# Optimization experiments

Hardware: AMD Instinct MI355X
Metric: run time of the kernel (lower is better)

Reference implementation:

```python
import jax, jax.numpy as jnp
import numpy as np

V, D, H, F, L, B, T = 32000, 512, 8, 2048, 4, 4, 1024
DK = D // H
S = 0.02  # init scale


def setup_inputs() -> dict:
    key = jax.random.key(0)
    ks = jax.random.split(key, 10)
    inp = {
        'x': jax.random.randint(ks[0], (B, T), 0, V),
        'embed': jax.random.normal(ks[1], (V, D), jnp.float32) * S,
        'Wq': jax.random.normal(ks[2], (L, D, D), jnp.float32) * S,
        'bq': jnp.zeros((L, D), jnp.float32),
        'Wk': jax.random.normal(ks[3], (L, D, D), jnp.float32) * S,
        'bk': jnp.zeros((L, D), jnp.float32),
        'Wv': jax.random.normal(ks[4], (L, D, D), jnp.float32) * S,
        'bv': jnp.zeros((L, D), jnp.float32),
        'Wo': jax.random.normal(ks[5], (L, D, D), jnp.float32) * S,
        'bo': jnp.zeros((L, D), jnp.float32),
        'ln1_s': jnp.ones((L, D), jnp.float32),
        'ln1_b': jnp.zeros((L, D), jnp.float32),
        'W1': jax.random.normal(ks[6], (L, D, F), jnp.float32) * S,
        'b1': jnp.zeros((L, F), jnp.float32),
        'W2': jax.random.normal(ks[7], (L, F, D), jnp.float32) * S,
        'b2': jnp.zeros((L, D), jnp.float32),
        'ln2_s': jnp.ones((L, D), jnp.float32),
        'ln2_b': jnp.zeros((L, D), jnp.float32),
        'lnf_s': jnp.ones((D,), jnp.float32),
        'lnf_b': jnp.zeros((D,), jnp.float32),
        'Wl': jax.random.normal(ks[8], (D, V), jnp.float32) * S,
        'bl': jnp.zeros((V,), jnp.float32),
    }
    return inp


def _layernorm(x, s, b, eps=1e-5):
    m = jnp.mean(x, axis=-1, keepdims=True)
    v = jnp.mean(jnp.square(x - m), axis=-1, keepdims=True)
    return (x - m) * jax.lax.rsqrt(v + eps) * s + b


def _forward(x, embed, Wq, bq, Wk, bk, Wv, bv, Wo, bo, ln1_s, ln1_b,
             W1, b1, W2, b2, ln2_s, ln2_b, lnf_s, lnf_b, Wl, bl):
    Bb, Tt = x.shape
    emb = embed.at[0].set(0.0)  # padding_idx = 0
    h = emb[x]  # [B,T,D]
    # sinusoidal positional encoding
    pos = jnp.arange(Tt, dtype=jnp.float32)[:, None]
    div = jnp.exp(jnp.arange(0, D, 2, dtype=jnp.float32) * (-np.log(10000.0) / D))
    pe = jnp.zeros((Tt, D), jnp.float32)
    pe = pe.at[:, 0::2].set(jnp.sin(pos * div)).at[:, 1::2].set(jnp.cos(pos * div))
    h = h + pe[None]
    # additive causal mask: 0 on/below diag, -inf above
    causal = jnp.triu(jnp.full((Tt, Tt), -jnp.inf, jnp.float32), 1)
    scale = 1.0 / np.sqrt(DK)
    for l in range(L):
        q = (h @ Wq[l] + bq[l]).reshape(Bb, Tt, H, DK)
        k = (h @ Wk[l] + bk[l]).reshape(Bb, Tt, H, DK)
        v = (h @ Wv[l] + bv[l]).reshape(Bb, Tt, H, DK)
        scores = jnp.einsum('bqhd,bkhd->bhqk', q, k) * scale + causal
        attn = jax.nn.softmax(scores, axis=-1)  # dropout=0 -> identity
        o = jnp.einsum('bhqk,bkhd->bqhd', attn, v).reshape(Bb, Tt, D)
        o = o @ Wo[l] + bo[l]
        h = _layernorm(h + o, ln1_s[l], ln1_b[l])
        ff = jax.nn.gelu(h @ W1[l] + b1[l], approximate=False) @ W2[l] + b2[l]
        h = _layernorm(h + ff, ln2_s[l], ln2_b[l])
    h = _layernorm(h, lnf_s, lnf_b)
    return h @ Wl + bl  # [B,T,V] logits


def reference(x, embed, Wq, bq, Wk, bk, Wv, bv, Wo, bo, ln1_s, ln1_b,
              W1, b1, W2, b2, ln2_s, ln2_b, lnf_s, lnf_b, Wl, bl):
    return _forward(x, embed, Wq, bq, Wk, bk, Wv, bv, Wo, bo, ln1_s, ln1_b,
                    W1, b1, W2, b2, ln2_s, ln2_b, lnf_s, lnf_b, Wl, bl)
```

## Files before the change

### kernel.cpp

```cpp
#include <hip/hip_runtime.h>
#include <math.h>

#define Mtot 4096
#define Dd   512
#define Hh   8
#define DKk  64
#define TT   1024
#define Ff   2048
#define Ll   4
#define Vv   32000

typedef __attribute__((ext_vector_type(8))) short bf16x8;
typedef __attribute__((ext_vector_type(4))) float f32x4;
typedef unsigned short u16;

__device__ __forceinline__ u16 f2b(float f) {
    union { float f; unsigned u; } x; x.f = f;
    unsigned r = x.u + 0x7fffu + ((x.u >> 16) & 1u);
    return (u16)(r >> 16);
}

typedef const __attribute__((address_space(1))) unsigned int* gp_t;
typedef __attribute__((address_space(3))) unsigned int* lp_t;
#define GLOAD_LDS16(g, l) __builtin_amdgcn_global_load_lds((gp_t)(const void*)(g), (lp_t)(void*)(l), 16, 0, 0)
#define SBAR  __builtin_amdgcn_s_barrier()
#define SCHED0 __builtin_amdgcn_sched_barrier(0)

#define SWZ(row, c)  ((c) ^ (((row) & 7) << 3))

__global__ __launch_bounds__(256) void embed_pe_kernel(const int* __restrict__ x,
                                                       const float* __restrict__ embed,
                                                       float* __restrict__ h,
                                                       u16* __restrict__ hb) {
    int idx = blockIdx.x * 256 + threadIdx.x;
    int d  = idx & (Dd - 1);
    int bt = idx >> 9;
    int t  = bt & (TT - 1);
    int tok = x[bt];
    float val = (tok == 0) ? 0.0f : embed[(size_t)tok * Dd + d];
    int de = d & ~1;
    float ang = (float)t * expf((float)de * (-9.210340371976184f / (float)Dd));
    val += (d & 1) ? cosf(ang) : sinf(ang);
    h[idx] = val;
    hb[idx] = f2b(val);
}

__global__ __launch_bounds__(256) void transpose_all(const float* __restrict__ Wq, const float* __restrict__ Wk,
                                                     const float* __restrict__ Wv, const float* __restrict__ Wo,
                                                     const float* __restrict__ W1, const float* __restrict__ W2,
                                                     const float* __restrict__ Wl,
                                                     u16* __restrict__ WqkvT, u16* __restrict__ WoT,
                                                     u16* __restrict__ W1T, u16* __restrict__ W2T,
                                                     u16* __restrict__ WlT) {
    __shared__ float t[32][33];
    int id = blockIdx.x;
    const float* src; u16* dst; int K, N, tx, ty;
    if (id < 12288) {
        int l = id / 3072, r = id - l * 3072;
        if (r < 768) {
            int which = r >> 8, t2 = r & 255;
            src = (which == 0 ? Wq : which == 1 ? Wk : Wv) + (size_t)l * 262144;
            dst = WqkvT + (size_t)l * 786432 + (size_t)which * 262144;
            K = 512; N = 512; ty = t2 >> 4; tx = t2 & 15;
        } else if (r < 1024) {
            int t2 = r - 768;
            src = Wo + (size_t)l * 262144; dst = WoT + (size_t)l * 262144;
            K = 512; N = 512; ty = t2 >> 4; tx = t2 & 15;
        } else if (r < 2048) {
            int t2 = r - 1024;
            src = W1 + (size_t)l * 1048576; dst = W1T + (size_t)l * 1048576;
            K = 512; N = 2048; ty = t2 >> 6; tx = t2 & 63;
        } else {
            int t2 = r - 2048;
            src = W2 + (size_t)l * 1048576; dst = W2T + (size_t)l * 1048576;
            K = 2048; N = 512; ty = t2 >> 4; tx = t2 & 15;
        }
    } else {
        int t2 = id - 12288;
        src = Wl; dst = WlT; K = 512; N = 32000;
        ty = t2 / 1000; tx = t2 - ty * 1000;
    }
    int n0 = tx * 32, k0 = ty * 32;
    int tid = threadIdx.x, c = tid & 31, rr = tid >> 5;
    #pragma unroll
    for (int i = 0; i < 4; i++)
        t[rr + i * 8][c] = src[(size_t)(k0 + rr + i * 8) * N + n0 + c];
    __syncthreads();
    #pragma unroll
    for (int i = 0; i < 4; i++)
        dst[(size_t)(n0 + rr + i * 8) * K + k0 + c] = f2b(t[c][rr + i * 8]);
}

__global__ __launch_bounds__(256) void biaspack_kernel(const float* __restrict__ bq,
                                                       const float* __restrict__ bk,
                                                       const float* __restrict__ bv,
                                                       float* __restrict__ bqkv) {
    int idx = blockIdx.x * 256 + threadIdx.x;
    int l = idx / 1536, j = idx - l * 1536;
    float v = (j < 512) ? bq[l * 512 + j] : (j < 1024) ? bk[l * 512 + j - 512] : bv[l * 512 + j - 1024];
    bqkv[idx] = v;
}

template<int ACT, int OUTB, int QKVMODE>
__global__ __launch_bounds__(256, 2) void mfma_gemm(const u16* __restrict__ A,
                                                    const u16* __restrict__ BT,
                                                    const float* __restrict__ bias,
                                                    float* __restrict__ outF,
                                                    u16* __restrict__ outB,
                                                    u16* __restrict__ vtb,
                                                    int M, int N, int K, int gx) {
    __shared__ __align__(16) u16 As[2][128 * 64];
    __shared__ __align__(16) u16 Bs[2][128 * 64];
    int tid = threadIdx.x;
    int lane = tid & 63, w = tid >> 6;
    int nwg = gridDim.x, flat = blockIdx.x;
    int wg = (flat & 7) * (nwg >> 3) + (flat >> 3);
    int bm = wg / gx, bn = wg - bm * gx;
    int wr = w >> 1, wc = w & 1;
    int fr = lane & 15, fq = lane >> 4;

    int sr = lane >> 3, sc = lane & 7;
    int scol = (sc ^ sr) * 8;
    const u16* Ab = A  + (size_t)(bm * 128 + w * 32 + sr) * K + scol;
    const u16* Bb = BT + (size_t)(bn * 128 + w * 32 + sr) * K + scol;
    u16* lA = &As[0][0] + w * 2048;
    u16* lB = &Bs[0][0] + w * 2048;

    f32x4 acc[4][4] = {};
    int nk = K >> 6;

#define STAGE(buf, kt)                                                     \
    {   int ko = (kt) * 64;                                                \
        GLOAD_LDS16(Ab + ko,          lA + (buf) * (128 * 64));            \
        GLOAD_LDS16(Ab + 8 * K + ko,  lA + (buf) * (128 * 64) + 512);      \
        GLOAD_LDS16(Ab + 16 * K + ko, lA + (buf) * (128 * 64) + 1024);     \
        GLOAD_LDS16(Ab + 24 * K + ko, lA + (buf) * (128 * 64) + 1536);     \
        GLOAD_LDS16(Bb + ko,          lB + (buf) * (128 * 64));            \
        GLOAD_LDS16(Bb + 8 * K + ko,  lB + (buf) * (128 * 64) + 512);      \
        GLOAD_LDS16(Bb + 16 * K + ko, lB + (buf) * (128 * 64) + 1024);     \
        GLOAD_LDS16(Bb + 24 * K + ko, lB + (buf) * (128 * 64) + 1536); }

    STAGE(0, 0);
    STAGE(1, 1);

    int cur = 0;
    for (int kt = 0; kt < nk; kt++) {
        if (kt + 1 < nk) { asm volatile("s_waitcnt vmcnt(8)" ::: "memory"); }
        else             { asm volatile("s_waitcnt vmcnt(0)" ::: "memory"); }
        SBAR;
        SCHED0;
        bf16x8 a[4][2], b[4][2];
        #pragma unroll
        for (int m = 0; m < 4; m++) {
            int row = wr * 64 + m * 16 + fr;
            a[m][0] = *(const bf16x8*)&As[cur][row * 64 + ((fq ^ (row & 7)) * 8)];
            a[m][1] = *(const bf16x8*)&As[cur][row * 64 + (((fq + 4) ^ (row & 7)) * 8)];
        }
        #pragma unroll
        for (int n = 0; n < 4; n++) {
            int row = wc * 64 + n * 16 + fr;
            b[n][0] = *(const bf16x8*)&Bs[cur][row * 64 + ((fq ^ (row & 7)) * 8)];
            b[n][1] = *(const bf16x8*)&Bs[cur][row * 64 + (((fq + 4) ^ (row & 7)) * 8)];
        }
        __builtin_amdgcn_s_setprio(1);
        #pragma unroll
        for (int m = 0; m < 4; m++)
            #pragma unroll
            for (int n = 0; n < 4; n++) {
                acc[m][n] = __builtin_amdgcn_mfma_f32_16x16x32_bf16(a[m][0], b[n][0], acc[m][n], 0, 0, 0);
                acc[m][n] = __builtin_amdgcn_mfma_f32_16x16x32_bf16(a[m][1], b[n][1], acc[m][n], 0, 0, 0);
            }
        __builtin_amdgcn_s_setprio(0);
        SCHED0;
        SBAR;
        SCHED0;
        if (kt + 2 < nk) STAGE(cur, kt + 2);
        cur ^= 1;
    }
#undef STAGE

    #pragma unroll
    for (int m = 0; m < 4; m++) {
        #pragma unroll
        for (int n = 0; n < 4; n++) {
            int col = bn * 128 + wc * 64 + n * 16 + fr;
            float bs = bias ? bias[col] : 0.0f;
            if (QKVMODE && bn >= 8) {
                int hh = (col - 1024) >> 6, d = (col - 1024) & 63;
                #pragma unroll
                for (int r = 0; r < 4; r++) {
                    int row = bm * 128 + wr * 64 + m * 16 + fq * 4 + r;
                    int bb = row >> 10, t = row & 1023;
                    vtb[(((size_t)bb * Hh + hh) * 64 + d) * 1024 + t] = f2b(acc[m][n][r] + bs);
                }
            } else {
                #pragma unroll
                for (int r = 0; r < 4; r++) {
                    int row = bm * 128 + wr * 64 + m * 16 + fq * 4 + r;
                    float v = acc[m][n][r] + bs;
                    if (ACT == 1) v = 0.5f * v * (1.0f + erff(v * 0.7071067811865475f));
                    if (OUTB) outB[(size_t)row * N + col] = f2b(v);
                    else      outF[(size_t)row * N + col] = v;
                }
            }
        }
    }
}

__global__ __launch_bounds__(512, 1) void mfma_gemm256(const u16* __restrict__ A,
                                                       const u16* __restrict__ BT,
                                                       const float* __restrict__ bias,
                                                       float* __restrict__ outF,
                                                       int M, int N, int K, int gy) {
    __shared__ __align__(16) u16 As[2][256 * 64];
    __shared__ __align__(16) u16 Bs[2][256 * 64];
    int tid = threadIdx.x;
    int lane = tid & 63, w = tid >> 6;
    int nwg = gridDim.x, flat = blockIdx.x;
    int wg = (flat & 7) * (nwg >> 3) + (flat >> 3);
    int bm = wg & (gy - 1), bn = wg >> 4;
    int wr = w >> 2, wc = w & 3;
    int fr = lane & 15, fq = lane >> 4;

    int sr8 = lane >> 3, sc = lane & 7;
    int scol = (sc ^ sr8) * 8;
    const u16* Ab = A  + (size_t)(bm * 256 + w * 32 + sr8) * K + scol;
    const u16* Bb = BT + (size_t)(bn * 256 + w * 32 + sr8) * K + scol;

    f32x4 acc[8][4] = {};
    int nk = K >> 6;

#define STAGE256(buf, kt)                                                    \
    {   int ko = (kt) * 64;                                                  \
        GLOAD_LDS16(Ab + ko,          &As[buf][(w * 32 +  0) * 64]);         \
        GLOAD_LDS16(Ab + 8 * K + ko,  &As[buf][(w * 32 +  8) * 64]);         \
        GLOAD_LDS16(Ab + 16 * K + ko, &As[buf][(w * 32 + 16) * 64]);         \
        GLOAD_LDS16(Ab + 24 * K + ko, &As[buf][(w * 32 + 24) * 64]);         \
        GLOAD_LDS16(Bb + ko,          &Bs[buf][(w * 32 +  0) * 64]);         \
        GLOAD_LDS16(Bb + 8 * K + ko,  &Bs[buf][(w * 32 +  8) * 64]);         \
        GLOAD_LDS16(Bb + 16 * K + ko, &Bs[buf][(w * 32 + 16) * 64]);         \
        GLOAD_LDS16(Bb + 24 * K + ko, &Bs[buf][(w * 32 + 24) * 64]); }

    STAGE256(0, 0);
    STAGE256(1, 1);

    int cur = 0;
    for (int kt = 0; kt < nk; kt++) {
        if (kt + 1 < nk) { asm volatile("s_waitcnt vmcnt(8)" ::: "memory"); }
        else             { asm volatile("s_waitcnt vmcnt(0)" ::: "memory"); }
        SBAR;
        SCHED0;
        bf16x8 b[4][2];
        #pragma unroll
        for (int n = 0; n < 4; n++) {
            int row = wc * 64 + n * 16 + fr;
            b[n][0] = *(const bf16x8*)&Bs[cur][row * 64 + ((fq ^ (row & 7)) * 8)];
            b[n][1] = *(const bf16x8*)&Bs[cur][row * 64 + (((fq + 4) ^ (row & 7)) * 8)];
        }
        #pragma unroll
        for (int m = 0; m < 8; m++) {
            int row = wr * 128 + m * 16 + fr;
            bf16x8 a0 = *(const bf16x8*)&As[cur][row * 64 + ((fq ^ (row & 7)) * 8)];
            bf16x8 a1 = *(const bf16x8*)&As[cur][row * 64 + (((fq + 4) ^ (row & 7)) * 8)];
            __builtin_amdgcn_s_setprio(1);
            #pragma unroll
            for (int n = 0; n < 4; n++) {
                acc[m][n] = __builtin_amdgcn_mfma_f32_16x16x32_bf16(a0, b[n][0], acc[m][n], 0, 0, 0);
                acc[m][n] = __builtin_amdgcn_mfma_f32_16x16x32_bf16(a1, b[n][1], acc[m][n], 0, 0, 0);
            }
            __builtin_amdgcn_s_setprio(0);
        }
        SCHED0;
        SBAR;
        SCHED0;
        if (kt + 2 < nk) STAGE256(cur, kt + 2);
        cur ^= 1;
    }
#undef STAGE256

    #pragma unroll
    for (int m = 0; m < 8; m++) {
        #pragma unroll
        for (int n = 0; n < 4; n++) {
            int col = bn * 256 + wc * 64 + n * 16 + fr;
            float bs = bias[col];
            #pragma unroll
            for (int r = 0; r < 4; r++) {
                int row = bm * 256 + wr * 128 + m * 16 + fq * 4 + r;
                outF[(size_t)row * N + col] = acc[m][n][r] + bs;
            }
        }
    }
}

__global__ __launch_bounds__(256) void attn_mfma(const u16* __restrict__ qkv,
                                                 const u16* __restrict__ vtb,
                                                 u16* __restrict__ ob) {
    int qt = (int)gridDim.x - 1 - (int)blockIdx.x;
    int hh = blockIdx.y, b = blockIdx.z;
    __shared__ __align__(16) u16 Qs[64 * 64];
    __shared__ __align__(16) u16 Ks[64 * 64];
    __shared__ __align__(16) u16 Vs[64 * 64];
    __shared__ __align__(16) u16 Ps[4][16 * 64];
    int tid = threadIdx.x;
    int lane = tid & 63, w = tid >> 6;
    int fr = lane & 15, fq = lane >> 4;
    int q0 = qt * 64;
    int sr = tid >> 2, sc0 = (tid & 3) * 16;

    bf16x8 rk0, rk1, rv0, rv1;
    bf16x8 sk0, sk1, sv0, sv1;

    auto load_a = [&](int kt) {
        const u16* srcK = qkv + ((size_t)(b * TT + kt * 64 + sr)) * 1536 + 512 + hh * 64 + sc0;
        rk0 = *(const bf16x8*)srcK; rk1 = *(const bf16x8*)(srcK + 8);
        const u16* srcV = vtb + (((size_t)(b * Hh + hh)) * 64 + sr) * 1024 + kt * 64 + sc0;
        rv0 = *(const bf16x8*)srcV; rv1 = *(const bf16x8*)(srcV + 8);
    };
    auto load_b = [&](int kt) {
        const u16* srcK = qkv + ((size_t)(b * TT + kt * 64 + sr)) * 1536 + 512 + hh * 64 + sc0;
        sk0 = *(const bf16x8*)srcK; sk1 = *(const bf16x8*)(srcK + 8);
        const u16* srcV = vtb + (((size_t)(b * Hh + hh)) * 64 + sr) * 1024 + kt * 64 + sc0;
        sv0 = *(const bf16x8*)srcV; sv1 = *(const bf16x8*)(srcV + 8);
    };
    auto store_a = [&]() {
        *(bf16x8*)&Ks[sr * 64 + SWZ(sr, sc0)]     = rk0;
        *(bf16x8*)&Ks[sr * 64 + SWZ(sr, sc0 + 8)] = rk1;
        *(bf16x8*)&Vs[sr * 64 + SWZ(sr, sc0)]     = rv0;
        *(bf16x8*)&Vs[sr * 64 + SWZ(sr, sc0 + 8)] = rv1;
    };
    auto store_b = [&]() {
        *(bf16x8*)&Ks[sr * 64 + SWZ(sr, sc0)]     = sk0;
        *(bf16x8*)&Ks[sr * 64 + SWZ(sr, sc0 + 8)] = sk1;
        *(bf16x8*)&Vs[sr * 64 + SWZ(sr, sc0)]     = sv0;
        *(bf16x8*)&Vs[sr * 64 + SWZ(sr, sc0 + 8)] = sv1;
    };

    load_a(0);
    {
        const u16* src = qkv + ((size_t)(b * TT + q0 + sr)) * 1536 + hh * 64 + sc0;
        bf16x8 v0 = *(const bf16x8*)src;
        bf16x8 v1 = *(const bf16x8*)(src + 8);
        *(bf16x8*)&Qs[sr * 64 + SWZ(sr, sc0)]     = v0;
        *(bf16x8*)&Qs[sr * 64 + SWZ(sr, sc0 + 8)] = v1;
    }
    __syncthreads();
    bf16x8 aq0 = *(const bf16x8*)&Qs[(w * 16 + fr) * 64 + SWZ(w * 16 + fr, fq * 8)];
    bf16x8 aq1 = *(const bf16x8*)&Qs[(w * 16 + fr) * 64 + SWZ(w * 16 + fr, 32 + fq * 8)];

    f32x4 oa[4] = {};
    float mreg[4], lreg[4];
    #pragma unroll
    for (int i = 0; i < 4; i++) { mreg[i] = -1e30f; lreg[i] = 0.0f; }

    auto compute_tile = [&](int kt) {
        f32x4 sa[4] = {};
        __builtin_amdgcn_s_setprio(1);
        #pragma unroll
        for (int nt = 0; nt < 4; nt++) {
            int krow = nt * 16 + fr;
            bf16x8 b0 = *(const bf16x8*)&Ks[krow * 64 + SWZ(krow, fq * 8)];
            bf16x8 b1 = *(const bf16x8*)&Ks[krow * 64 + SWZ(krow, 32 + fq * 8)];
            sa[nt] = __builtin_amdgcn_mfma_f32_16x16x32_bf16(aq0, b0, sa[nt], 0, 0, 0);
            sa[nt] = __builtin_amdgcn_mfma_f32_16x16x32_bf16(aq1, b1, sa[nt], 0, 0, 0);
        }
        __builtin_amdgcn_s_setprio(0);

        float p[4][4];
        int qg = w * 16 + fq * 4;
        bool diag = (kt == qt);
        #pragma unroll
        for (int nt = 0; nt < 4; nt++)
            #pragma unroll
            for (int i = 0; i < 4; i++) {
                float s = sa[nt][i] * 0.125f;
                if (diag && (nt * 16 + fr > qg + i)) s = -1e30f;
                p[nt][i] = s;
            }

        float mnew[4], fscale[4];
        #pragma unroll
        for (int i = 0; i < 4; i++) {
            float v = fmaxf(fmaxf(p[0][i], p[1][i]), fmaxf(p[2][i], p[3][i]));
            v = fmaxf(v, __shfl_xor(v, 1));
            v = fmaxf(v, __shfl_xor(v, 2));
            v = fmaxf(v, __shfl_xor(v, 4));
            v = fmaxf(v, __shfl_xor(v, 8));
            mnew[i] = fmaxf(mreg[i], v);
            fscale[i] = __expf(mreg[i] - mnew[i]);
            mreg[i] = mnew[i];
        }
        #pragma unroll
        for (int i = 0; i < 4; i++) {
            float sum = 0.f;
            #pragma unroll
            for (int nt = 0; nt < 4; nt++) {
                float e = __expf(p[nt][i] - mnew[i]);
                p[nt][i] = e;
                sum += e;
            }
            sum += __shfl_xor(sum, 1);
            sum += __shfl_xor(sum, 2);
            sum += __shfl_xor(sum, 4);
            sum += __shfl_xor(sum, 8);
            lreg[i] = lreg[i] * fscale[i] + sum;
        }
        #pragma unroll
        for (int nn = 0; nn < 4; nn++)
            #pragma unroll
            for (int i = 0; i < 4; i++)
                oa[nn][i] *= fscale[i];

        u16* ps = &Ps[w][0];
        #pragma unroll
        for (int nt = 0; nt < 4; nt++)
            #pragma unroll
            for (int i = 0; i < 4; i++) {
                int row = fq * 4 + i, col = nt * 16 + fr;
                ps[row * 64 + SWZ(row, col)] = f2b(p[nt][i]);
            }
        bf16x8 pa0 = *(const bf16x8*)&ps[fr * 64 + SWZ(fr, fq * 8)];
        bf16x8 pa1 = *(const bf16x8*)&ps[fr * 64 + SWZ(fr, 32 + fq * 8)];
        __builtin_amdgcn_s_setprio(1);
        #pragma unroll
        for (int nn = 0; nn < 4; nn++) {
            int drow = nn * 16 + fr;
            bf16x8 vb0 = *(const bf16x8*)&Vs[drow * 64 + SWZ(drow, fq * 8)];
            bf16x8 vb1 = *(const bf16x8*)&Vs[drow * 64 + SWZ(drow, 32 + fq * 8)];
            oa[nn] = __builtin_amdgcn_mfma_f32_16x16x32_bf16(pa0, vb0, oa[nn], 0, 0, 0);
            oa[nn] = __builtin_amdgcn_mfma_f32_16x16x32_bf16(pa1, vb1, oa[nn], 0, 0, 0);
        }
        __builtin_amdgcn_s_setprio(0);
    };

    int kt = 0;
    for (;;) {
        SCHED0; SBAR;
        store_a();
        if (kt + 1 <= qt) load_b(kt + 1);
        asm volatile("s_waitcnt lgkmcnt(0)" ::: "memory");
        SBAR; SCHED0;
        compute_tile(kt);
        if (++kt > qt) break;

        SCHED0; SBAR;
        store_b();
        if (kt + 1 <= qt) load_a(kt + 1);
        asm volatile("s_waitcnt lgkmcnt(0)" ::: "memory");
        SBAR; SCHED0;
        compute_tile(kt);
        if (++kt > qt) break;
    }

    #pragma unroll
    for (int i = 0; i < 4; i++) {
        float inv = 1.0f / lreg[i];
        size_t row = (size_t)(b * TT + q0 + w * 16 + fq * 4 + i) * Dd + hh * 64;
        #pragma unroll
        for (int nn = 0; nn < 4; nn++)
            ob[row + nn * 16 + fr] = f2b(oa[nn][i] * inv);
    }
}

__global__ __launch_bounds__(256) void ln_kernel(float* __restrict__ h,
                                                 const float* __restrict__ d1,
                                                 const float* __restrict__ gs,
                                                 const float* __restrict__ gb,
                                                 u16* __restrict__ hb) {
    int w = threadIdx.x >> 6, lane = threadIdx.x & 63;
    int row = (blockIdx.x << 2) + w;
    size_t base = (size_t)row * Dd + lane * 8;
    f32x4 v0 = *(const f32x4*)&h[base];
    f32x4 v1 = *(const f32x4*)&h[base + 4];
    if (d1) { v0 += *(const f32x4*)&d1[base]; v1 += *(const f32x4*)&d1[base + 4]; }
    float s = v0[0] + v0[1] + v0[2] + v0[3] + v1[0] + v1[1] + v1[2] + v1[3];
    #pragma unroll
    for (int st = 1; st < 64; st <<= 1) s += __shfl_xor(s, st);
    float m = s * (1.0f / Dd);
    float q = 0.f;
    #pragma unroll
    for (int j = 0; j < 4; j++) { float a = v0[j] - m, b = v1[j] - m; q += a * a + b * b; }
    #pragma unroll
    for (int st = 1; st < 64; st <<= 1) q += __shfl_xor(q, st);
    float r = rsqrtf(q * (1.0f / Dd) + 1e-5f);
    f32x4 g0 = *(const f32x4*)&gs[lane * 8],     g1 = *(const f32x4*)&gs[lane * 8 + 4];
    f32x4 c0 = *(const f32x4*)&gb[lane * 8],     c1 = *(const f32x4*)&gb[lane * 8 + 4];
    f32x4 y0, y1;
    bf16x8 yb;
    #pragma unroll
    for (int j = 0; j < 4; j++) {
        y0[j] = (v0[j] - m) * r * g0[j] + c0[j];
        y1[j] = (v1[j] - m) * r * g1[j] + c1[j];
        yb[j]     = (short)f2b(y0[j]);
        yb[j + 4] = (short)f2b(y1[j]);
    }
    *(f32x4*)&h[base]     = y0;
    *(f32x4*)&h[base + 4] = y1;
    *(bf16x8*)&hb[base]   = yb;
}

extern "C" void kernel_launch(void* const* d_in, const int* in_sizes, int n_in,
                              void* d_out, int out_size, void* d_ws, size_t ws_size,
                              hipStream_t stream) {
    const int*   x     = (const int*)  d_in[0];
    const float* embed = (const float*)d_in[1];
    const float* Wq    = (const float*)d_in[2];
    const float* bq    = (const float*)d_in[3];
    const float* Wk    = (const float*)d_in[4];
    const float* bk    = (const float*)d_in[5];
    const float* Wv    = (const float*)d_in[6];
    const float* bv    = (const float*)d_in[7];
    const float* Wo    = (const float*)d_in[8];
    const float* bo    = (const float*)d_in[9];
    const float* ln1_s = (const float*)d_in[10];
    const float* ln1_b = (const float*)d_in[11];
    const float* W1    = (const float*)d_in[12];
    const float* b1    = (const float*)d_in[13];
    const float* W2    = (const float*)d_in[14];
    const float* b2    = (const float*)d_in[15];
    const float* ln2_s = (const float*)d_in[16];
    const float* ln2_b = (const float*)d_in[17];
    const float* lnf_s = (const float*)d_in[18];
    const float* lnf_b = (const float*)d_in[19];
    const float* Wl    = (const float*)d_in[20];
    const float* bl    = (const float*)d_in[21];

    char* wp = (char*)d_ws;
    float* h    = (float*)wp;  wp += (size_t)Mtot * Dd * 4;
    float* pb   = (float*)wp;  wp += (size_t)Mtot * Dd * 4;
    u16*   hb   = (u16*)wp;    wp += (size_t)Mtot * Dd * 2;
    u16*   qkvb = (u16*)wp;    wp += (size_t)Mtot * 1536 * 2;
    u16*   vtb  = (u16*)wp;    wp += (size_t)Mtot * Dd * 2;
    u16*   obb  = (u16*)wp;    wp += (size_t)Mtot * Dd * 2;
    u16*   fbb  = (u16*)wp;    wp += (size_t)Mtot * Ff * 2;
    u16*   WlT  = (u16*)wp;    wp += (size_t)Vv * Dd * 2;
    float* bqkv = (float*)wp;  wp += (size_t)Ll * 1536 * 4;

    char* op = (char*)d_out;
    u16* WqkvT = (u16*)op;  op += (size_t)Ll * 1536 * Dd * 2;
    u16* WoT   = (u16*)op;  op += (size_t)Ll * Dd * Dd * 2;
    u16* W1T   = (u16*)op;  op += (size_t)Ll * Ff * Dd * 2;
    u16* W2T   = (u16*)op;  op += (size_t)Ll * Dd * Ff * 2;

    transpose_all<<<28288, 256, 0, stream>>>(Wq, Wk, Wv, Wo, W1, W2, Wl, WqkvT, WoT, W1T, W2T, WlT);
    biaspack_kernel<<<24, 256, 0, stream>>>(bq, bk, bv, bqkv);
    embed_pe_kernel<<<(Mtot * Dd) / 256, 256, 0, stream>>>(x, embed, h, hb);

    for (int l = 0; l < Ll; l++) {
        mfma_gemm<0, 1, 1><<<(1536 / 128) * (Mtot / 128), 256, 0, stream>>>(
            hb, WqkvT + (size_t)l * 1536 * Dd, bqkv + l * 1536, nullptr, qkvb, vtb,
            Mtot, 1536, Dd, 1536 / 128);
        attn_mfma<<<dim3(TT / 64, Hh, 4), 256, 0, stream>>>(qkvb, vtb, obb);
        mfma_gemm<0, 0, 0><<<(Dd / 128) * (Mtot / 128), 256, 0, stream>>>(
            obb, WoT + (size_t)l * Dd * Dd, bo + l * Dd, pb, nullptr, nullptr,
            Mtot, Dd, Dd, Dd / 128);
        ln_kernel<<<Mtot / 4, 256, 0, stream>>>(h, pb, ln1_s + l * Dd, ln1_b + l * Dd, hb);
        mfma_gemm<1, 1, 0><<<(Ff / 128) * (Mtot / 128), 256, 0, stream>>>(
            hb, W1T + (size_t)l * Ff * Dd, b1 + l * Ff, nullptr, fbb, nullptr,
            Mtot, Ff, Dd, Ff / 128);
        mfma_gemm<0, 0, 0><<<(Dd / 128) * (Mtot / 128), 256, 0, stream>>>(
            fbb, W2T + (size_t)l * Dd * Ff, b2 + l * Dd, pb, nullptr, nullptr,
            Mtot, Dd, Ff, Dd / 128);
        ln_kernel<<<Mtot / 4, 256, 0, stream>>>(h, pb, ln2_s + l * Dd, ln2_b + l * Dd, hb);
    }

    ln_kernel<<<Mtot / 4, 256, 0, stream>>>(h, nullptr, lnf_s, lnf_b, hb);
    mfma_gemm256<<<(Vv / 256) * (Mtot / 256), 512, 0, stream>>>(
        hb, WlT, bl, (float*)d_out, Mtot, Vv, Dd, Mtot / 256);
}
```

Before: 821.1 us.

## Split-K the Wo and W2 GEMMs and merge prep kernels into one launch

```diff
diff --git a/kernel.cpp b/kernel.cpp
--- a/kernel.cpp
+++ b/kernel.cpp
@@ -28,32 +28,40 @@
 
 #define SWZ(row, c)  ((c) ^ (((row) & 7) << 3))
 
-__global__ __launch_bounds__(256) void embed_pe_kernel(const int* __restrict__ x,
-                                                       const float* __restrict__ embed,
-                                                       float* __restrict__ h,
-                                                       u16* __restrict__ hb) {
-    int idx = blockIdx.x * 256 + threadIdx.x;
-    int d  = idx & (Dd - 1);
-    int bt = idx >> 9;
-    int t  = bt & (TT - 1);
-    int tok = x[bt];
-    float val = (tok == 0) ? 0.0f : embed[(size_t)tok * Dd + d];
-    int de = d & ~1;
-    float ang = (float)t * expf((float)de * (-9.210340371976184f / (float)Dd));
-    val += (d & 1) ? cosf(ang) : sinf(ang);
-    h[idx] = val;
-    hb[idx] = f2b(val);
-}
-
-__global__ __launch_bounds__(256) void transpose_all(const float* __restrict__ Wq, const float* __restrict__ Wk,
-                                                     const float* __restrict__ Wv, const float* __restrict__ Wo,
-                                                     const float* __restrict__ W1, const float* __restrict__ W2,
-                                                     const float* __restrict__ Wl,
-                                                     u16* __restrict__ WqkvT, u16* __restrict__ WoT,
-                                                     u16* __restrict__ W1T, u16* __restrict__ W2T,
-                                                     u16* __restrict__ WlT) {
+__global__ __launch_bounds__(256) void prep_kernel(const float* __restrict__ Wq, const float* __restrict__ Wk,
+                                                   const float* __restrict__ Wv, const float* __restrict__ Wo,
+                                                   const float* __restrict__ W1, const float* __restrict__ W2,
+                                                   const float* __restrict__ Wl,
+                                                   u16* __restrict__ WqkvT, u16* __restrict__ WoT,
+                                                   u16* __restrict__ W1T, u16* __restrict__ W2T,
+                                                   u16* __restrict__ WlT,
+                                                   const float* __restrict__ bq, const float* __restrict__ bk,
+                                                   const float* __restrict__ bv, float* __restrict__ bqkv,
+                                                   const int* __restrict__ x, const float* __restrict__ emw,
+                                                   float* __restrict__ h, u16* __restrict__ hb) {
+    int id = blockIdx.x;
+    if (id >= 28312) {
+        int idx = (id - 28312) * 256 + threadIdx.x;
+        int d  = idx & (Dd - 1);
+        int bt = idx >> 9;
+        int t  = bt & (TT - 1);
+        int tok = x[bt];
+        float val = (tok == 0) ? 0.0f : emw[(size_t)tok * Dd + d];
+        int de = d & ~1;
+        float ang = (float)t * expf((float)de * (-9.210340371976184f / (float)Dd));
+        val += (d & 1) ? cosf(ang) : sinf(ang);
+        h[idx] = val;
+        hb[idx] = f2b(val);
+        return;
+    }
+    if (id >= 28288) {
+        int idx = (id - 28288) * 256 + threadIdx.x;
+        int l = idx / 1536, j = idx - l * 1536;
+        float v = (j < 512) ? bq[l * 512 + j] : (j < 1024) ? bk[l * 512 + j - 512] : bv[l * 512 + j - 1024];
+        bqkv[idx] = v;
+        return;
+    }
     __shared__ float t[32][33];
-    int id = blockIdx.x;
     const float* src; u16* dst; int K, N, tx, ty;
     if (id < 12288) {
         int l = id / 3072, r = id - l * 3072;
@@ -91,43 +99,39 @@
         dst[(size_t)(n0 + rr + i * 8) * K + k0 + c] = f2b(t[c][rr + i * 8]);
 }
 
-__global__ __launch_bounds__(256) void biaspack_kernel(const float* __restrict__ bq,
-                                                       const float* __restrict__ bk,
-                                                       const float* __restrict__ bv,
-                                                       float* __restrict__ bqkv) {
-    int idx = blockIdx.x * 256 + threadIdx.x;
-    int l = idx / 1536, j = idx - l * 1536;
-    float v = (j < 512) ? bq[l * 512 + j] : (j < 1024) ? bk[l * 512 + j - 512] : bv[l * 512 + j - 1024];
-    bqkv[idx] = v;
-}
-
-template<int ACT, int OUTB, int QKVMODE>
+template<int ACT, int OUTB, int QKVMODE, int SPLITK>
 __global__ __launch_bounds__(256, 2) void mfma_gemm(const u16* __restrict__ A,
                                                     const u16* __restrict__ BT,
                                                     const float* __restrict__ bias,
                                                     float* __restrict__ outF,
                                                     u16* __restrict__ outB,
                                                     u16* __restrict__ vtb,
-                                                    int M, int N, int K, int gx) {
+                                                    int M, int N, int K, int gx, int PS) {
     __shared__ __align__(16) u16 As[2][128 * 64];
     __shared__ __align__(16) u16 Bs[2][128 * 64];
     int tid = threadIdx.x;
     int lane = tid & 63, w = tid >> 6;
     int nwg = gridDim.x, flat = blockIdx.x;
     int wg = (flat & 7) * (nwg >> 3) + (flat >> 3);
-    int bm = wg / gx, bn = wg - bm * gx;
+    int ks = 0, sub = wg;
+    if (SPLITK > 1) {
+        int tps = gx * (M >> 7);
+        ks = wg / tps; sub = wg - ks * tps;
+    }
+    int bm = sub / gx, bn = sub - bm * gx;
+    int kb = ks * (K / SPLITK);
     int wr = w >> 1, wc = w & 1;
     int fr = lane & 15, fq = lane >> 4;
 
     int sr = lane >> 3, sc = lane & 7;
     int scol = (sc ^ sr) * 8;
-    const u16* Ab = A  + (size_t)(bm * 128 + w * 32 + sr) * K + scol;
-    const u16* Bb = BT + (size_t)(bn * 128 + w * 32 + sr) * K + scol;
+    const u16* Ab = A  + (size_t)(bm * 128 + w * 32 + sr) * K + kb + scol;
+    const u16* Bb = BT + (size_t)(bn * 128 + w * 32 + sr) * K + kb + scol;
     u16* lA = &As[0][0] + w * 2048;
     u16* lB = &Bs[0][0] + w * 2048;
 
     f32x4 acc[4][4] = {};
-    int nk = K >> 6;
+    int nk = (K / SPLITK) >> 6;
 
 #define STAGE(buf, kt)                                                     \
     {   int ko = (kt) * 64;                                                \
@@ -184,7 +188,7 @@
         #pragma unroll
         for (int n = 0; n < 4; n++) {
             int col = bn * 128 + wc * 64 + n * 16 + fr;
-            float bs = bias ? bias[col] : 0.0f;
+            float bs = (bias && ks == 0) ? bias[col] : 0.0f;
             if (QKVMODE && bn >= 8) {
                 int hh = (col - 1024) >> 6, d = (col - 1024) & 63;
                 #pragma unroll
@@ -200,7 +204,7 @@
                     float v = acc[m][n][r] + bs;
                     if (ACT == 1) v = 0.5f * v * (1.0f + erff(v * 0.7071067811865475f));
                     if (OUTB) outB[(size_t)row * N + col] = f2b(v);
-                    else      outF[(size_t)row * N + col] = v;
+                    else      outF[(size_t)ks * PS + (size_t)row * N + col] = v;
                 }
             }
         }
@@ -463,16 +467,21 @@
 }
 
 __global__ __launch_bounds__(256) void ln_kernel(float* __restrict__ h,
-                                                 const float* __restrict__ d1,
+                                                 const float* __restrict__ pp, int np,
                                                  const float* __restrict__ gs,
                                                  const float* __restrict__ gb,
                                                  u16* __restrict__ hb) {
     int w = threadIdx.x >> 6, lane = threadIdx.x & 63;
     int row = (blockIdx.x << 2) + w;
     size_t base = (size_t)row * Dd + lane * 8;
+    const size_t PART = (size_t)Mtot * Dd;
     f32x4 v0 = *(const f32x4*)&h[base];
     f32x4 v1 = *(const f32x4*)&h[base + 4];
-    if (d1) { v0 += *(const f32x4*)&d1[base]; v1 += *(const f32x4*)&d1[base + 4]; }
+    for (int p = 0; p < np; p++) {
+        const float* d = pp + (size_t)p * PART;
+        v0 += *(const f32x4*)&d[base];
+        v1 += *(const f32x4*)&d[base + 4];
+    }
     float s = v0[0] + v0[1] + v0[2] + v0[3] + v1[0] + v1[1] + v1[2] + v1[3];
     #pragma unroll
     for (int st = 1; st < 64; st <<= 1) s += __shfl_xor(s, st);
@@ -527,7 +536,6 @@
 
     char* wp = (char*)d_ws;
     float* h    = (float*)wp;  wp += (size_t)Mtot * Dd * 4;
-    float* pb   = (float*)wp;  wp += (size_t)Mtot * Dd * 4;
     u16*   hb   = (u16*)wp;    wp += (size_t)Mtot * Dd * 2;
     u16*   qkvb = (u16*)wp;    wp += (size_t)Mtot * 1536 * 2;
     u16*   vtb  = (u16*)wp;    wp += (size_t)Mtot * Dd * 2;
@@ -541,30 +549,33 @@
     u16* WoT   = (u16*)op;  op += (size_t)Ll * Dd * Dd * 2;
     u16* W1T   = (u16*)op;  op += (size_t)Ll * Ff * Dd * 2;
     u16* W2T   = (u16*)op;  op += (size_t)Ll * Dd * Ff * 2;
-
-    transpose_all<<<28288, 256, 0, stream>>>(Wq, Wk, Wv, Wo, W1, W2, Wl, WqkvT, WoT, W1T, W2T, WlT);
-    biaspack_kernel<<<24, 256, 0, stream>>>(bq, bk, bv, bqkv);
-    embed_pe_kernel<<<(Mtot * Dd) / 256, 256, 0, stream>>>(x, embed, h, hb);
+    float* pbx = (float*)op; op += (size_t)4 * Mtot * Dd * 4;
+
+    prep_kernel<<<36504, 256, 0, stream>>>(Wq, Wk, Wv, Wo, W1, W2, Wl,
+                                           WqkvT, WoT, W1T, W2T, WlT,
+                                           bq, bk, bv, bqkv, x, embed, h, hb);
+
+    const int PS = Mtot * Dd;
 
     for (int l = 0; l < Ll; l++) {
-        mfma_gemm<0, 1, 1><<<(1536 / 128) * (Mtot / 128), 256, 0, stream>>>(
+        mfma_gemm<0, 1, 1, 1><<<(1536 / 128) * (Mtot / 128), 256, 0, stream>>>(
             hb, WqkvT + (size_t)l * 1536 * Dd, bqkv + l * 1536, nullptr, qkvb, vtb,
-            Mtot, 1536, Dd, 1536 / 128);
+            Mtot, 1536, Dd, 1536 / 128, 0);
         attn_mfma<<<dim3(TT / 64, Hh, 4), 256, 0, stream>>>(qkvb, vtb, obb);
-        mfma_gemm<0, 0, 0><<<(Dd / 128) * (Mtot / 128), 256, 0, stream>>>(
-            obb, WoT + (size_t)l * Dd * Dd, bo + l * Dd, pb, nullptr, nullptr,
-            Mtot, Dd, Dd, Dd / 128);
-        ln_kernel<<<Mtot / 4, 256, 0, stream>>>(h, pb, ln1_s + l * Dd, ln1_b + l * Dd, hb);
-        mfma_gemm<1, 1, 0><<<(Ff / 128) * (Mtot / 128), 256, 0, stream>>>(
+        mfma_gemm<0, 0, 0, 2><<<2 * (Dd / 128) * (Mtot / 128), 256, 0, stream>>>(
+            obb, WoT + (size_t)l * Dd * Dd, bo + l * Dd, pbx, nullptr, nullptr,
+            Mtot, Dd, Dd, Dd / 128, PS);
+        ln_kernel<<<Mtot / 4, 256, 0, stream>>>(h, pbx, 2, ln1_s + l * Dd, ln1_b + l * Dd, hb);
+        mfma_gemm<1, 1, 0, 1><<<(Ff / 128) * (Mtot / 128), 256, 0, stream>>>(
             hb, W1T + (size_t)l * Ff * Dd, b1 + l * Ff, nullptr, fbb, nullptr,
-            Mtot, Ff, Dd, Ff / 128);
-        mfma_gemm<0, 0, 0><<<(Dd / 128) * (Mtot / 128), 256, 0, stream>>>(
-            fbb, W2T + (size_t)l * Dd * Ff, b2 + l * Dd, pb, nullptr, nullptr,
-            Mtot, Dd, Ff, Dd / 128);
-        ln_kernel<<<Mtot / 4, 256, 0, stream>>>(h, pb, ln2_s + l * Dd, ln2_b + l * Dd, hb);
-    }
-
-    ln_kernel<<<Mtot / 4, 256, 0, stream>>>(h, nullptr, lnf_s, lnf_b, hb);
+            Mtot, Ff, Dd, Ff / 128, 0);
+        mfma_gemm<0, 0, 0, 4><<<4 * (Dd / 128) * (Mtot / 128), 256, 0, stream>>>(
+            fbb, W2T + (size_t)l * Dd * Ff, b2 + l * Dd, pbx, nullptr, nullptr,
+            Mtot, Dd, Ff, Dd / 128, PS);
+        ln_kernel<<<Mtot / 4, 256, 0, stream>>>(h, pbx, 4, ln2_s + l * Dd, ln2_b + l * Dd, hb);
+    }
+
+    ln_kernel<<<Mtot / 4, 256, 0, stream>>>(h, nullptr, 0, lnf_s, lnf_b, hb);
     mfma_gemm256<<<(Vv / 256) * (Mtot / 256), 512, 0, stream>>>(
         hb, WlT, bl, (float*)d_out, Mtot, Vv, Dd, Mtot / 256);
 }
```

New measurement: 759.6 us. -7.5%, faster.
